# Performance work log

Measured on AMD Instinct MI355X. Metric: run time of the kernel, lower is better.

## Reference

```python
import jax, jax.numpy as jnp
import numpy as np

B, C, IC, H, W = 2, 64, 32, 96, 96


def setup_inputs() -> dict:
    key = jax.random.key(0)
    ks = jax.random.split(key, 8)
    s_in = 1.0 / np.sqrt(C)
    s_ic = 1.0 / np.sqrt(IC)
    return {
        "x": jax.random.normal(ks[0], (B, C, H, W), dtype=jnp.float32),
        "Wg": jax.random.uniform(ks[1], (IC, C), jnp.float32, -s_in, s_in),
        "bg": jax.random.uniform(ks[2], (IC,), jnp.float32, -s_in, s_in),
        "Wt": jax.random.uniform(ks[3], (IC, C), jnp.float32, -s_in, s_in),
        "bt": jax.random.uniform(ks[4], (IC,), jnp.float32, -s_in, s_in),
        "Wp": jax.random.uniform(ks[5], (IC, C), jnp.float32, -s_in, s_in),
        "bp": jax.random.uniform(ks[6], (IC,), jnp.float32, -s_in, s_in),
        "Wo": jax.random.uniform(ks[7], (C, IC), jnp.float32, -s_ic, s_ic),
        "bo": jax.random.uniform(jax.random.fold_in(key, 9), (C,), jnp.float32, -s_ic, s_ic),
    }


def reference(x, Wg, bg, Wt, bt, Wp, bp, Wo, bo):
    b, c, h, w = x.shape
    n = h * w
    xf = x.reshape(b, c, n)  # [B, C, N]

    def proj(Wc, bc):  # 1x1 conv == channel GEMM -> [B, IC, N]
        return jnp.einsum("bcn,oc->bon", xf, Wc) + bc[None, :, None]

    g = proj(Wg, bg)
    theta = proj(Wt, bt)
    phi = proj(Wp, bp)
    scores = jnp.einsum("bcn,bcm->bnm", theta, phi)  # [B, N, N]
    att = jax.nn.softmax(scores, axis=-1)
    y = jnp.einsum("bnm,bcm->bcn", att, g)  # [B, IC, N]
    o = jnp.einsum("bcn,oc->bon", y, Wo) + bo[None, :, None]  # [B, C, N]
    return o.reshape(b, c, h, w) + x
```

## Files before the change

kernel.cpp:

```cpp
#include <hip/hip_runtime.h>
#include <hip/hip_bf16.h>


#define B_   2
#define C_   64
#define IC_  32
#define N_   9216
#define QBLK128    72
#define LOG2E 1.44269504088896f

typedef __attribute__((ext_vector_type(2))) float  f32x2;
typedef __attribute__((ext_vector_type(4))) float  f32x4;
typedef __attribute__((ext_vector_type(8))) short  s16x8;

static __device__ __forceinline__ ushort f2bf(float f) {
  union { __hip_bfloat16 h; ushort u; } cv;
  cv.h = __float2bfloat16(f);
  return cv.u;
}

static __device__ __forceinline__ float bf2f(ushort u) {
  union { uint i; float f; } c;
  c.i = ((uint)u) << 16;
  return c.f;
}

static __device__ __forceinline__ f32x4 mfma32(s16x8 a, s16x8 b, f32x4 c) {
  return __builtin_amdgcn_mfma_f32_16x16x32_bf16(a, b, c, 0, 0, 0);
}

__global__ __launch_bounds__(256) void proj_kernel(
    const float* __restrict__ x,
    const float* __restrict__ Wg, const float* __restrict__ bg,
    const float* __restrict__ Wt, const float* __restrict__ bt,
    const float* __restrict__ Wp, const float* __restrict__ bp,
    ushort* __restrict__ Qb, ushort* __restrict__ Kb, ushort* __restrict__ Vt)
{
  const int grp = blockIdx.x / 36;
  const int ic0 = grp * 8;
  const int bn0 = (blockIdx.x % 36) * 512 + threadIdx.x * 2;
  const int b   = bn0 / N_;
  const int n   = bn0 % N_;

  float ag[8][2], at_[8][2], ap[8][2];
#pragma unroll
  for (int j = 0; j < 8; ++j)
#pragma unroll
    for (int k = 0; k < 2; ++k) { ag[j][k] = 0.f; at_[j][k] = 0.f; ap[j][k] = 0.f; }

  const float* xp = x + (size_t)b * C_ * N_ + n;
#pragma unroll 4
  for (int c = 0; c < C_; ++c) {
    const f32x2 xv = *reinterpret_cast<const f32x2*>(xp + (size_t)c * N_);
#pragma unroll
    for (int j = 0; j < 8; ++j) {
      const float wg = Wg[(ic0 + j) * C_ + c];
      const float wt = Wt[(ic0 + j) * C_ + c];
      const float wp = Wp[(ic0 + j) * C_ + c];
#pragma unroll
      for (int k = 0; k < 2; ++k) {
        ag[j][k]  = fmaf(wg, xv[k], ag[j][k]);
        at_[j][k] = fmaf(wt, xv[k], at_[j][k]);
        ap[j][k]  = fmaf(wp, xv[k], ap[j][k]);
      }
    }
  }

#pragma unroll
  for (int k = 0; k < 2; ++k) {
    const int bn = bn0 + k, nn = n + k;
    union { ushort u[8]; s16x8 v; } qv, kv;
#pragma unroll
    for (int j = 0; j < 8; ++j) {
      const int ic = ic0 + j;
      qv.u[j] = f2bf(LOG2E * (at_[j][k] + bt[ic]));
      kv.u[j] = f2bf(ap[j][k] + bp[ic]);
    }
    *reinterpret_cast<s16x8*>(Qb + (size_t)bn * IC_ + ic0) = qv.v;
    *reinterpret_cast<s16x8*>(Kb + (size_t)bn * IC_ + ic0) = kv.v;
    const int j6 = nn & 63, u = j6 >> 5, r = j6 & 31;
    const int nperm = (nn - j6) + u * 32 + (r & 15) * 2 + (r >> 4);
#pragma unroll
    for (int j = 0; j < 8; ++j) {
      const int ic = ic0 + j;
      Vt[(size_t)(b * IC_ + ic) * N_ + nperm] = f2bf(ag[j][k] + bg[ic]);
    }
  }
}

template<int NSEG>
__global__ __launch_bounds__(256, 4) void attn_kernel(
    const ushort* __restrict__ Qb, const ushort* __restrict__ Kb,
    const ushort* __restrict__ Vt, ushort* __restrict__ Opart,
    float* __restrict__ Lp)
{
  constexpr int NT = 144 / NSEG;
  constexpr int SKEYS = N_ / NSEG;
  constexpr int KSTR = 36;
  constexpr int VSTR = 70;
  __shared__ __align__(16) ushort Kl[64 * KSTR];
  __shared__ __align__(16) ushort Vl[32 * VSTR];

  const int qblk = blockIdx.x % QBLK128;
  const int bs   = blockIdx.x / QBLK128;
  const int seg  = bs % NSEG;
  const int b    = bs / NSEG;
  const int key0 = seg * SKEYS;

  const int tid  = threadIdx.x;
  const int lane = tid & 63;
  const int wave = tid >> 6;
  const int q16  = lane & 15;
  const int h    = lane >> 4;

  const int qbaseA = qblk * 128 + wave * 32;
  const int qbaseB = qbaseA + 16;

  const short ONE = (short)0x3F80;
  const s16x8 ones = {ONE, ONE, ONE, ONE, ONE, ONE, ONE, ONE};

  const s16x8 qfragA = *reinterpret_cast<const s16x8*>(
      Qb + (size_t)(b * N_ + qbaseA + q16) * IC_ + h * 8);
  const s16x8 qfragB = *reinterpret_cast<const s16x8*>(
      Qb + (size_t)(b * N_ + qbaseB + q16) * IC_ + h * 8);

  f32x4 aA0 = {0.f,0.f,0.f,0.f}, aA1 = {0.f,0.f,0.f,0.f}, aLA = {0.f,0.f,0.f,0.f};
  f32x4 aB0 = {0.f,0.f,0.f,0.f}, aB1 = {0.f,0.f,0.f,0.f}, aLB = {0.f,0.f,0.f,0.f};

  const int krow = tid >> 2, kpart = tid & 3;
  const ushort* kg = Kb + ((size_t)b * N_ + key0 + krow) * IC_ + kpart * 8;
  ushort* kl_dst = &Kl[krow * KSTR + kpart * 8];

  const int vd = tid >> 3, vp = tid & 7;
  const ushort* vg = Vt + (size_t)(b * IC_ + vd) * N_ + key0 + vp * 8;
  ushort* vl_dst = &Vl[vd * VSTR + vp * 8];

  s16x8 kreg = *reinterpret_cast<const s16x8*>(kg);
  s16x8 vreg = *reinterpret_cast<const s16x8*>(vg);

  for (int it = 0; it < NT; ++it) {
    *reinterpret_cast<s16x8*>(kl_dst) = kreg;
    *reinterpret_cast<s16x8*>(vl_dst) = vreg;
    __syncthreads();

    if (it + 1 < NT) {
      kg += 64 * IC_;
      vg += 64;
      kreg = *reinterpret_cast<const s16x8*>(kg);
      vreg = *reinterpret_cast<const s16x8*>(vg);
    }

#pragma unroll
    for (int u = 0; u < 2; ++u) {
      const s16x8 kf0 = *reinterpret_cast<const s16x8*>(&Kl[(u * 32 + q16) * KSTR + h * 8]);
      const s16x8 kf1 = *reinterpret_cast<const s16x8*>(&Kl[(u * 32 + 16 + q16) * KSTR + h * 8]);
      const f32x4 z = {0.f, 0.f, 0.f, 0.f};
      const f32x4 sA0 = mfma32(kf0, qfragA, z);
      const f32x4 sA1 = mfma32(kf1, qfragA, z);
      const f32x4 sB0 = mfma32(kf0, qfragB, z);
      const f32x4 sB1 = mfma32(kf1, qfragB, z);

      const s16x8 vf0 = *reinterpret_cast<const s16x8*>(&Vl[q16 * VSTR + u * 32 + h * 8]);
      const s16x8 vf1 = *reinterpret_cast<const s16x8*>(&Vl[(16 + q16) * VSTR + u * 32 + h * 8]);

      union { ushort us[8]; s16x8 v; } paA, paB;
#pragma unroll
      for (int i = 0; i < 4; ++i) {
        paA.us[2 * i]     = f2bf(__builtin_amdgcn_exp2f(sA0[i]));
        paA.us[2 * i + 1] = f2bf(__builtin_amdgcn_exp2f(sA1[i]));
        paB.us[2 * i]     = f2bf(__builtin_amdgcn_exp2f(sB0[i]));
        paB.us[2 * i + 1] = f2bf(__builtin_amdgcn_exp2f(sB1[i]));
      }
      aA0 = mfma32(paA.v, vf0, aA0);
      aA1 = mfma32(paA.v, vf1, aA1);
      aLA = mfma32(paA.v, ones, aLA);
      aB0 = mfma32(paB.v, vf0, aB0);
      aB1 = mfma32(paB.v, vf1, aB1);
      aLB = mfma32(paB.v, ones, aLB);
    }
    __syncthreads();
  }

  const size_t obase0 = ((size_t)(b * NSEG + seg) * N_);
#pragma unroll
  for (int r = 0; r < 4; ++r) {
    const int qA = qbaseA + h * 4 + r;
    const int qB = qbaseB + h * 4 + r;
    Opart[(obase0 + qA) * IC_ + q16]      = f2bf(aA0[r]);
    Opart[(obase0 + qA) * IC_ + 16 + q16] = f2bf(aA1[r]);
    Opart[(obase0 + qB) * IC_ + q16]      = f2bf(aB0[r]);
    Opart[(obase0 + qB) * IC_ + 16 + q16] = f2bf(aB1[r]);
  }
  if (q16 == 0) {
#pragma unroll
    for (int r = 0; r < 4; ++r) {
      Lp[obase0 + qbaseA + h * 4 + r] = aLA[r];
      Lp[obase0 + qbaseB + h * 4 + r] = aLB[r];
    }
  }
}

template<int NSEG>
__global__ __launch_bounds__(256) void combine_kernel(
    const ushort* __restrict__ Opart, const float* __restrict__ Lp,
    ushort* __restrict__ Y)
{
  const int idx     = blockIdx.x * 256 + threadIdx.x;
  const int bn      = idx >> 2;
  const int quarter = idx & 3;
  const int b       = bn / N_;
  const int q       = bn % N_;

  float l = 0.f;
  float o[8];
#pragma unroll
  for (int j = 0; j < 8; ++j) o[j] = 0.f;

#pragma unroll
  for (int s = 0; s < NSEG; ++s) {
    const size_t base = (size_t)(b * NSEG + s) * N_ + q;
    l += Lp[base];
    union { s16x8 v; ushort us[8]; } ov;
    ov.v = *reinterpret_cast<const s16x8*>(Opart + base * IC_ + quarter * 8);
#pragma unroll
    for (int j = 0; j < 8; ++j) o[j] += bf2f(ov.us[j]);
  }
  const float inv = 1.0f / l;
  union { ushort us[8]; s16x8 v; } yv;
#pragma unroll
  for (int j = 0; j < 8; ++j) yv.us[j] = f2bf(o[j] * inv);
  *reinterpret_cast<s16x8*>(Y + (size_t)bn * IC_ + quarter * 8) = yv.v;
}

__global__ __launch_bounds__(256) void out_kernel(
    const ushort* __restrict__ Y, const float* __restrict__ Wo,
    const float* __restrict__ bo, const float* __restrict__ x,
    float* __restrict__ out)
{
  const int g    = blockIdx.x / 72;
  const int oc0  = g * 16;
  const int bn   = (blockIdx.x % 72) * 256 + threadIdx.x;
  const int b    = bn / N_;
  const int n    = bn % N_;

  float yv[32];
#pragma unroll
  for (int i = 0; i < 4; ++i) {
    union { s16x8 v; ushort us[8]; } ov;
    ov.v = *reinterpret_cast<const s16x8*>(Y + (size_t)bn * IC_ + i * 8);
#pragma unroll
    for (int j = 0; j < 8; ++j) yv[i * 8 + j] = bf2f(ov.us[j]);
  }

  float acc[16];
#pragma unroll
  for (int j = 0; j < 16; ++j) acc[j] = bo[oc0 + j];

#pragma unroll
  for (int ic = 0; ic < IC_; ++ic) {
    const float yv_ic = yv[ic];
#pragma unroll
    for (int j = 0; j < 16; ++j)
      acc[j] = fmaf(Wo[(oc0 + j) * IC_ + ic], yv_ic, acc[j]);
  }

#pragma unroll
  for (int j = 0; j < 16; ++j) {
    const int oc = oc0 + j;
    const size_t xi = (size_t)(b * C_ + oc) * N_ + n;
    out[xi] = acc[j] + x[xi];
  }
}

extern "C" void kernel_launch(void* const* d_in, const int* in_sizes, int n_in,
                              void* d_out, int out_size, void* d_ws, size_t ws_size,
                              hipStream_t stream)
{
  const float* x  = (const float*)d_in[0];
  const float* Wg = (const float*)d_in[1];
  const float* bg = (const float*)d_in[2];
  const float* Wt = (const float*)d_in[3];
  const float* bt = (const float*)d_in[4];
  const float* Wp = (const float*)d_in[5];
  const float* bp = (const float*)d_in[6];
  const float* Wo = (const float*)d_in[7];
  const float* bo = (const float*)d_in[8];
  float* out = (float*)d_out;

  char* ws = (char*)d_ws;
  const size_t szb = (size_t)B_ * N_ * IC_ * sizeof(ushort);
  ushort* Qb = (ushort*)(ws);
  ushort* Kb = (ushort*)(ws + szb);
  ushort* Vt = (ushort*)(ws + 2 * szb);
  ushort* Op = (ushort*)(ws + 3 * szb);
  ushort* Yb = (ushort*)(ws);

  const size_t need16 = 3 * szb + 16 * szb + (size_t)16 * B_ * N_ * sizeof(float);

  proj_kernel<<<144, 256, 0, stream>>>(x, Wg, bg, Wt, bt, Wp, bp, Qb, Kb, Vt);
  if (ws_size >= need16) {
    float* Lp = (float*)(ws + 3 * szb + 16 * szb);
    attn_kernel<16><<<B_ * 16 * QBLK128, 256, 0, stream>>>(Qb, Kb, Vt, Op, Lp);
    combine_kernel<16><<<(B_ * N_ * 4) / 256, 256, 0, stream>>>(Op, Lp, Yb);
  } else {
    float* Lp = (float*)(ws + 3 * szb + 8 * szb);
    attn_kernel<8><<<B_ * 8 * QBLK128, 256, 0, stream>>>(Qb, Kb, Vt, Op, Lp);
    combine_kernel<8><<<(B_ * N_ * 4) / 256, 256, 0, stream>>>(Op, Lp, Yb);
  }
  out_kernel<<<4 * 72, 256, 0, stream>>>(Yb, Wo, bo, x, out);
}
```

Baseline: 80.89 us.

## Raise parallelism in proj/combine/out kernels and batch attention MFMAs with setprio

The projection kernel now computes one position per thread with twice the blocks. The combine kernel uses 8 threads per query instead of 4, and the output kernel handles 8 output channels per block instead of 16, doubling their grids. In the attention inner loop, the two 32-key halves are merged so that all eight score MFMAs are issued back-to-back, then all exponentials, then the PV and row-sum MFMAs, each MFMA group wrapped in s_setprio. This aims to fill the GPU better in the small kernels and to improve MFMA/VALU overlap in attention, at the cost of more register pressure and more redundant x and weight loads.

```diff
diff --git a/kernel.cpp b/kernel.cpp
--- a/kernel.cpp
+++ b/kernel.cpp
@@ -9,9 +9,9 @@
 #define QBLK128    72
 #define LOG2E 1.44269504088896f
 
-typedef __attribute__((ext_vector_type(2))) float  f32x2;
 typedef __attribute__((ext_vector_type(4))) float  f32x4;
 typedef __attribute__((ext_vector_type(8))) short  s16x8;
+typedef __attribute__((ext_vector_type(4))) short  s16x4;
 
 static __device__ __forceinline__ ushort f2bf(float f) {
   union { __hip_bfloat16 h; ushort u; } cv;
@@ -36,55 +36,44 @@
     const float* __restrict__ Wp, const float* __restrict__ bp,
     ushort* __restrict__ Qb, ushort* __restrict__ Kb, ushort* __restrict__ Vt)
 {
-  const int grp = blockIdx.x / 36;
+  const int grp = blockIdx.x / 72;
   const int ic0 = grp * 8;
-  const int bn0 = (blockIdx.x % 36) * 512 + threadIdx.x * 2;
-  const int b   = bn0 / N_;
-  const int n   = bn0 % N_;
-
-  float ag[8][2], at_[8][2], ap[8][2];
-#pragma unroll
-  for (int j = 0; j < 8; ++j)
-#pragma unroll
-    for (int k = 0; k < 2; ++k) { ag[j][k] = 0.f; at_[j][k] = 0.f; ap[j][k] = 0.f; }
+  const int bn  = (blockIdx.x % 72) * 256 + threadIdx.x;
+  const int b   = bn / N_;
+  const int n   = bn % N_;
+
+  float ag[8], at_[8], ap[8];
+#pragma unroll
+  for (int j = 0; j < 8; ++j) { ag[j] = 0.f; at_[j] = 0.f; ap[j] = 0.f; }
 
   const float* xp = x + (size_t)b * C_ * N_ + n;
-#pragma unroll 4
+#pragma unroll 8
   for (int c = 0; c < C_; ++c) {
-    const f32x2 xv = *reinterpret_cast<const f32x2*>(xp + (size_t)c * N_);
+    const float xv = xp[(size_t)c * N_];
 #pragma unroll
     for (int j = 0; j < 8; ++j) {
-      const float wg = Wg[(ic0 + j) * C_ + c];
-      const float wt = Wt[(ic0 + j) * C_ + c];
-      const float wp = Wp[(ic0 + j) * C_ + c];
-#pragma unroll
-      for (int k = 0; k < 2; ++k) {
-        ag[j][k]  = fmaf(wg, xv[k], ag[j][k]);
-        at_[j][k] = fmaf(wt, xv[k], at_[j][k]);
-        ap[j][k]  = fmaf(wp, xv[k], ap[j][k]);
-      }
+      ag[j]  = fmaf(Wg[(ic0 + j) * C_ + c], xv, ag[j]);
+      at_[j] = fmaf(Wt[(ic0 + j) * C_ + c], xv, at_[j]);
+      ap[j]  = fmaf(Wp[(ic0 + j) * C_ + c], xv, ap[j]);
     }
   }
 
-#pragma unroll
-  for (int k = 0; k < 2; ++k) {
-    const int bn = bn0 + k, nn = n + k;
-    union { ushort u[8]; s16x8 v; } qv, kv;
-#pragma unroll
-    for (int j = 0; j < 8; ++j) {
-      const int ic = ic0 + j;
-      qv.u[j] = f2bf(LOG2E * (at_[j][k] + bt[ic]));
-      kv.u[j] = f2bf(ap[j][k] + bp[ic]);
-    }
-    *reinterpret_cast<s16x8*>(Qb + (size_t)bn * IC_ + ic0) = qv.v;
-    *reinterpret_cast<s16x8*>(Kb + (size_t)bn * IC_ + ic0) = kv.v;
-    const int j6 = nn & 63, u = j6 >> 5, r = j6 & 31;
-    const int nperm = (nn - j6) + u * 32 + (r & 15) * 2 + (r >> 4);
-#pragma unroll
-    for (int j = 0; j < 8; ++j) {
-      const int ic = ic0 + j;
-      Vt[(size_t)(b * IC_ + ic) * N_ + nperm] = f2bf(ag[j][k] + bg[ic]);
-    }
+  union { ushort u[8]; s16x8 v; } qv, kv;
+#pragma unroll
+  for (int j = 0; j < 8; ++j) {
+    const int ic = ic0 + j;
+    qv.u[j] = f2bf(LOG2E * (at_[j] + bt[ic]));
+    kv.u[j] = f2bf(ap[j] + bp[ic]);
+  }
+  *reinterpret_cast<s16x8*>(Qb + (size_t)bn * IC_ + ic0) = qv.v;
+  *reinterpret_cast<s16x8*>(Kb + (size_t)bn * IC_ + ic0) = kv.v;
+
+  const int j6 = n & 63, u = j6 >> 5, r = j6 & 31;
+  const int nperm = (n - j6) + u * 32 + (r & 15) * 2 + (r >> 4);
+#pragma unroll
+  for (int j = 0; j < 8; ++j) {
+    const int ic = ic0 + j;
+    Vt[(size_t)(b * IC_ + ic) * N_ + nperm] = f2bf(ag[j] + bg[ic]);
   }
 }
 
@@ -150,34 +139,53 @@
       vreg = *reinterpret_cast<const s16x8*>(vg);
     }
 
-#pragma unroll
-    for (int u = 0; u < 2; ++u) {
-      const s16x8 kf0 = *reinterpret_cast<const s16x8*>(&Kl[(u * 32 + q16) * KSTR + h * 8]);
-      const s16x8 kf1 = *reinterpret_cast<const s16x8*>(&Kl[(u * 32 + 16 + q16) * KSTR + h * 8]);
-      const f32x4 z = {0.f, 0.f, 0.f, 0.f};
-      const f32x4 sA0 = mfma32(kf0, qfragA, z);
-      const f32x4 sA1 = mfma32(kf1, qfragA, z);
-      const f32x4 sB0 = mfma32(kf0, qfragB, z);
-      const f32x4 sB1 = mfma32(kf1, qfragB, z);
-
-      const s16x8 vf0 = *reinterpret_cast<const s16x8*>(&Vl[q16 * VSTR + u * 32 + h * 8]);
-      const s16x8 vf1 = *reinterpret_cast<const s16x8*>(&Vl[(16 + q16) * VSTR + u * 32 + h * 8]);
-
-      union { ushort us[8]; s16x8 v; } paA, paB;
-#pragma unroll
-      for (int i = 0; i < 4; ++i) {
-        paA.us[2 * i]     = f2bf(__builtin_amdgcn_exp2f(sA0[i]));
-        paA.us[2 * i + 1] = f2bf(__builtin_amdgcn_exp2f(sA1[i]));
-        paB.us[2 * i]     = f2bf(__builtin_amdgcn_exp2f(sB0[i]));
-        paB.us[2 * i + 1] = f2bf(__builtin_amdgcn_exp2f(sB1[i]));
-      }
-      aA0 = mfma32(paA.v, vf0, aA0);
-      aA1 = mfma32(paA.v, vf1, aA1);
-      aLA = mfma32(paA.v, ones, aLA);
-      aB0 = mfma32(paB.v, vf0, aB0);
-      aB1 = mfma32(paB.v, vf1, aB1);
-      aLB = mfma32(paB.v, ones, aLB);
+    const s16x8 kf00 = *reinterpret_cast<const s16x8*>(&Kl[(q16)      * KSTR + h * 8]);
+    const s16x8 kf01 = *reinterpret_cast<const s16x8*>(&Kl[(16 + q16) * KSTR + h * 8]);
+    const s16x8 kf10 = *reinterpret_cast<const s16x8*>(&Kl[(32 + q16) * KSTR + h * 8]);
+    const s16x8 kf11 = *reinterpret_cast<const s16x8*>(&Kl[(48 + q16) * KSTR + h * 8]);
+    const f32x4 z = {0.f, 0.f, 0.f, 0.f};
+    __builtin_amdgcn_s_setprio(1);
+    const f32x4 sA0 = mfma32(kf00, qfragA, z);
+    const f32x4 sA1 = mfma32(kf01, qfragA, z);
+    const f32x4 sB0 = mfma32(kf00, qfragB, z);
+    const f32x4 sB1 = mfma32(kf01, qfragB, z);
+    const f32x4 sA2 = mfma32(kf10, qfragA, z);
+    const f32x4 sA3 = mfma32(kf11, qfragA, z);
+    const f32x4 sB2 = mfma32(kf10, qfragB, z);
+    const f32x4 sB3 = mfma32(kf11, qfragB, z);
+    __builtin_amdgcn_s_setprio(0);
+
+    union { ushort us[8]; s16x8 v; } paA0, paA1, paB0, paB1;
+#pragma unroll
+    for (int i = 0; i < 4; ++i) {
+      paA0.us[2 * i]     = f2bf(__builtin_amdgcn_exp2f(sA0[i]));
+      paA0.us[2 * i + 1] = f2bf(__builtin_amdgcn_exp2f(sA1[i]));
+      paA1.us[2 * i]     = f2bf(__builtin_amdgcn_exp2f(sA2[i]));
+      paA1.us[2 * i + 1] = f2bf(__builtin_amdgcn_exp2f(sA3[i]));
+      paB0.us[2 * i]     = f2bf(__builtin_amdgcn_exp2f(sB0[i]));
+      paB0.us[2 * i + 1] = f2bf(__builtin_amdgcn_exp2f(sB1[i]));
+      paB1.us[2 * i]     = f2bf(__builtin_amdgcn_exp2f(sB2[i]));
+      paB1.us[2 * i + 1] = f2bf(__builtin_amdgcn_exp2f(sB3[i]));
     }
+
+    const s16x8 vf00 = *reinterpret_cast<const s16x8*>(&Vl[q16 * VSTR + h * 8]);
+    const s16x8 vf01 = *reinterpret_cast<const s16x8*>(&Vl[(16 + q16) * VSTR + h * 8]);
+    const s16x8 vf10 = *reinterpret_cast<const s16x8*>(&Vl[q16 * VSTR + 32 + h * 8]);
+    const s16x8 vf11 = *reinterpret_cast<const s16x8*>(&Vl[(16 + q16) * VSTR + 32 + h * 8]);
+    __builtin_amdgcn_s_setprio(1);
+    aA0 = mfma32(paA0.v, vf00, aA0);
+    aA1 = mfma32(paA0.v, vf01, aA1);
+    aB0 = mfma32(paB0.v, vf00, aB0);
+    aB1 = mfma32(paB0.v, vf01, aB1);
+    aA0 = mfma32(paA1.v, vf10, aA0);
+    aA1 = mfma32(paA1.v, vf11, aA1);
+    aB0 = mfma32(paB1.v, vf10, aB0);
+    aB1 = mfma32(paB1.v, vf11, aB1);
+    aLA = mfma32(paA0.v, ones, aLA);
+    aLA = mfma32(paA1.v, ones, aLA);
+    aLB = mfma32(paB0.v, ones, aLB);
+    aLB = mfma32(paB1.v, ones, aLB);
+    __builtin_amdgcn_s_setprio(0);
     __syncthreads();
   }
 
@@ -205,31 +213,31 @@
     const ushort* __restrict__ Opart, const float* __restrict__ Lp,
     ushort* __restrict__ Y)
 {
-  const int idx     = blockIdx.x * 256 + threadIdx.x;
-  const int bn      = idx >> 2;
-  const int quarter = idx & 3;
-  const int b       = bn / N_;
-  const int q       = bn % N_;
+  const int idx = blockIdx.x * 256 + threadIdx.x;
+  const int bn  = idx >> 3;
+  const int e   = idx & 7;
+  const int b   = bn / N_;
+  const int q   = bn % N_;
 
   float l = 0.f;
-  float o[8];
-#pragma unroll
-  for (int j = 0; j < 8; ++j) o[j] = 0.f;
+  float o[4];
+#pragma unroll
+  for (int j = 0; j < 4; ++j) o[j] = 0.f;
 
 #pragma unroll
   for (int s = 0; s < NSEG; ++s) {
     const size_t base = (size_t)(b * NSEG + s) * N_ + q;
     l += Lp[base];
-    union { s16x8 v; ushort us[8]; } ov;
-    ov.v = *reinterpret_cast<const s16x8*>(Opart + base * IC_ + quarter * 8);
-#pragma unroll
-    for (int j = 0; j < 8; ++j) o[j] += bf2f(ov.us[j]);
+    union { s16x4 v; ushort us[4]; } ov;
+    ov.v = *reinterpret_cast<const s16x4*>(Opart + base * IC_ + e * 4);
+#pragma unroll
+    for (int j = 0; j < 4; ++j) o[j] += bf2f(ov.us[j]);
   }
   const float inv = 1.0f / l;
-  union { ushort us[8]; s16x8 v; } yv;
-#pragma unroll
-  for (int j = 0; j < 8; ++j) yv.us[j] = f2bf(o[j] * inv);
-  *reinterpret_cast<s16x8*>(Y + (size_t)bn * IC_ + quarter * 8) = yv.v;
+  union { ushort us[4]; s16x4 v; } yv;
+#pragma unroll
+  for (int j = 0; j < 4; ++j) yv.us[j] = f2bf(o[j] * inv);
+  *reinterpret_cast<s16x4*>(Y + (size_t)bn * IC_ + e * 4) = yv.v;
 }
 
 __global__ __launch_bounds__(256) void out_kernel(
@@ -238,7 +246,7 @@
     float* __restrict__ out)
 {
   const int g    = blockIdx.x / 72;
-  const int oc0  = g * 16;
+  const int oc0  = g * 8;
   const int bn   = (blockIdx.x % 72) * 256 + threadIdx.x;
   const int b    = bn / N_;
   const int n    = bn % N_;
@@ -252,20 +260,20 @@
     for (int j = 0; j < 8; ++j) yv[i * 8 + j] = bf2f(ov.us[j]);
   }
 
-  float acc[16];
-#pragma unroll
-  for (int j = 0; j < 16; ++j) acc[j] = bo[oc0 + j];
+  float acc[8];
+#pragma unroll
+  for (int j = 0; j < 8; ++j) acc[j] = bo[oc0 + j];
 
 #pragma unroll
   for (int ic = 0; ic < IC_; ++ic) {
     const float yv_ic = yv[ic];
 #pragma unroll
-    for (int j = 0; j < 16; ++j)
+    for (int j = 0; j < 8; ++j)
       acc[j] = fmaf(Wo[(oc0 + j) * IC_ + ic], yv_ic, acc[j]);
   }
 
 #pragma unroll
-  for (int j = 0; j < 16; ++j) {
+  for (int j = 0; j < 8; ++j) {
     const int oc = oc0 + j;
     const size_t xi = (size_t)(b * C_ + oc) * N_ + n;
     out[xi] = acc[j] + x[xi];
@@ -297,15 +305,15 @@
 
   const size_t need16 = 3 * szb + 16 * szb + (size_t)16 * B_ * N_ * sizeof(float);
 
-  proj_kernel<<<144, 256, 0, stream>>>(x, Wg, bg, Wt, bt, Wp, bp, Qb, Kb, Vt);
+  proj_kernel<<<288, 256, 0, stream>>>(x, Wg, bg, Wt, bt, Wp, bp, Qb, Kb, Vt);
   if (ws_size >= need16) {
     float* Lp = (float*)(ws + 3 * szb + 16 * szb);
     attn_kernel<16><<<B_ * 16 * QBLK128, 256, 0, stream>>>(Qb, Kb, Vt, Op, Lp);
-    combine_kernel<16><<<(B_ * N_ * 4) / 256, 256, 0, stream>>>(Op, Lp, Yb);
+    combine_kernel<16><<<(B_ * N_ * 8) / 256, 256, 0, stream>>>(Op, Lp, Yb);
   } else {
     float* Lp = (float*)(ws + 3 * szb + 8 * szb);
     attn_kernel<8><<<B_ * 8 * QBLK128, 256, 0, stream>>>(Qb, Kb, Vt, Op, Lp);
-    combine_kernel<8><<<(B_ * N_ * 4) / 256, 256, 0, stream>>>(Op, Lp, Yb);
-  }
-  out_kernel<<<4 * 72, 256, 0, stream>>>(Yb, Wo, bo, x, out);
-}
+    combine_kernel<8><<<(B_ * N_ * 8) / 256, 256, 0, stream>>>(Op, Lp, Yb);
+  }
+  out_kernel<<<8 * 72, 256, 0, stream>>>(Yb, Wo, bo, x, out);
+}
```

After: 75.57 us. 6.6% less time.
